# Performance work log

Hardware: AMD Instinct MI355X
Metric: run time of the kernel (lower is better)

The kernel has to match this reference:

```python
import jax, jax.numpy as jnp
import numpy as np

L = 4096
E = 512   # embed dim
S = 1024  # state dim
H = 150   # Scorer hidden dim
GI = 2 * S + E
MAX_N = 10


def _scorer(x, W1, b1, W2, b2, W3, b3):
    h = jax.nn.relu(x @ W1 + b1)
    h = jax.nn.relu(h @ W2 + b2)
    return h @ W3 + b3  # [..., 1]


def setup_inputs() -> dict:
    key = jax.random.key(0)
    ks = jax.random.split(key, 16)
    def init(k, shape, fan_in):
        return jax.random.normal(k, shape, dtype=jnp.float32) / np.sqrt(fan_in)
    inp = {
        "embeds": jax.random.normal(ks[0], (L, E), dtype=jnp.float32),
        "states": jax.random.normal(ks[1], (L, S), dtype=jnp.float32),
        # attention Scorer params (input S)
        "aW1": init(ks[2], (S, H), S), "ab1": jnp.zeros((H,), jnp.float32),
        "aW2": init(ks[3], (H, H), H), "ab2": jnp.zeros((H,), jnp.float32),
        "aW3": init(ks[4], (H, 1), H), "ab3": jnp.zeros((1,), jnp.float32),
        # sm Scorer params (input GI)
        "sW1": init(ks[5], (GI, H), GI), "sb1": jnp.zeros((H,), jnp.float32),
        "sW2": init(ks[6], (H, H), H), "sb2": jnp.zeros((H,), jnp.float32),
        "sW3": init(ks[7], (H, 1), H), "sb3": jnp.zeros((1,), jnp.float32),
    }
    return inp


def reference(embeds, states, aW1, ab1, aW2, ab2, aW3, ab3,
              sW1, sb1, sW2, sb2, sW3, sb3):
    # per-token attention logits, computed once: [L]
    attns = _scorer(states, aW1, ab1, aW2, ab2, aW3, ab3)[:, 0]

    gs = []
    for n in range(1, MAX_N + 1):  # fixed small loop over window sizes
        M = L - n + 1                                  # number of windows
        starts = jnp.arange(M)
        idx = starts[:, None] + jnp.arange(n)          # [M, n] token indices
        w = jax.nn.softmax(attns[idx], axis=1)         # windowed softmax [M, n]
        pooled = jnp.einsum('mn,mne->me', w, embeds[idx])  # [M, E]
        g = jnp.concatenate([states[starts], states[starts + n - 1], pooled],
                            axis=1)                    # [M, 2S+E]
        gs.append(g)
    x = jnp.concatenate(gs, axis=0)                    # [T, GI], T = 10L-45
    scores = _scorer(x, sW1, sb1, sW2, sb2, sW3, sb3)[:, 0]  # [T]
    return scores
```

## Files before the change

kernel.cpp:

```cpp
#include <hip/hip_runtime.h>
#include <math.h>

#define LTOK 4096
#define EDIM 512
#define SDIM 1024
#define HDIM 150
#define SEG 160
#define MAXN 10
#define TOTAL_ROWS 40915
#define KA 1536
#define NKT 48
#define K2 160
#define NCG 42

typedef _Float16 hfrag __attribute__((ext_vector_type(8)));
typedef float ffrag __attribute__((ext_vector_type(4)));

#define MFMA_(a, b, c) __builtin_amdgcn_mfma_f32_16x16x32_f16(a, b, c, 0, 0, 0)


#define ITEMS_A   (LTOK * (KA / 8))
#define ITEMS_W   (NCG * NKT * 64)
#define ITEMS_W2  (K2 * (K2 / 8))
#define ITEMS_A2  (K2 * (K2 / 8))
#define ITEMS_TOT (ITEMS_A + ITEMS_W + ITEMS_W2 + ITEMS_A2)

__global__ __launch_bounds__(256) void prep_kernel(
    const float* __restrict__ embeds, const float* __restrict__ states,
    const float* __restrict__ aW1, const float* __restrict__ aW2,
    const float* __restrict__ sW1, const float* __restrict__ sW2,
    _Float16* __restrict__ Apk, _Float16* __restrict__ Wpk,
    _Float16* __restrict__ W2pk, _Float16* __restrict__ A2pk)
{
    int it = blockIdx.x * 256 + threadIdx.x;
    if (it < ITEMS_A) {
        const int rem = it % (NKT * 64);
        const int g = it / (NKT * 64), kt = rem >> 6, lane = rem & 63;
        const int row = g * 16 + (lane & 15);
        const int k0 = kt * 32 + (lane >> 4) * 8;
        const float* src = (k0 < SDIM) ? (states + (size_t)row * SDIM + k0)
                                       : (embeds + (size_t)row * EDIM + (k0 - SDIM));
        const float4 v0 = *(const float4*)src;
        const float4 v1 = *(const float4*)(src + 4);
        _Float16 o[8] = {(_Float16)v0.x, (_Float16)v0.y, (_Float16)v0.z, (_Float16)v0.w,
                         (_Float16)v1.x, (_Float16)v1.y, (_Float16)v1.z, (_Float16)v1.w};
        *(uint4*)(Apk + (size_t)it * 8) = *(uint4*)o;
        return;
    }
    it -= ITEMS_A;
    if (it < ITEMS_W) {
        const int rem = it % (NKT * 64);
        const int cgi = it / (NKT * 64), kt = rem >> 6, lane = rem & 63;
        const int col = cgi * 16 + (lane & 15);
        const int k0 = kt * 32 + (lane >> 4) * 8;
        _Float16 o[8];
        for (int j = 0; j < 8; ++j) {
            const int k = k0 + j;
            float wv = 0.f;
            if (col < 160) {
                if (col < HDIM && k < SDIM) wv = sW1[(size_t)k * HDIM + col];
            } else if (col < 320) {
                const int cj = col - 160;
                if (cj < HDIM && k < SDIM) wv = sW1[(size_t)(SDIM + k) * HDIM + cj];
            } else if (col < 480) {
                const int cj = col - 320;
                if (cj < HDIM && k >= SDIM) wv = sW1[(size_t)(SDIM + k) * HDIM + cj];
            } else if (col >= 512) {
                const int cj = col - 512;
                if (cj < HDIM && k < SDIM) wv = aW1[(size_t)k * HDIM + cj];
            }
            o[j] = (_Float16)wv;
        }
        *(uint4*)(Wpk + ((size_t)((size_t)cgi * NKT + kt) * 64 + lane) * 8) = *(uint4*)o;
        return;
    }
    it -= ITEMS_W;
    if (it < ITEMS_W2 + ITEMS_A2) {
        const bool is_a = (it >= ITEMS_W2);
        const int li = is_a ? (it - ITEMS_W2) : it;
        const float* src = is_a ? aW2 : sW2;
        _Float16* dst = is_a ? A2pk : W2pk;
        const int tk = li >> 6, lane = li & 63;
        const int col = (tk / 5) * 16 + (lane & 15);
        const int k0 = (tk % 5) * 32 + (lane >> 4) * 8;
        _Float16 o[8];
        for (int j = 0; j < 8; ++j) {
            const int k = k0 + j;
            float wv = (col < HDIM && k < HDIM) ? src[(size_t)k * HDIM + col] : 0.f;
            o[j] = (_Float16)wv;
        }
        *(uint4*)(dst + ((size_t)tk * 64 + lane) * 8) = *(uint4*)o;
    }
}

__global__ __launch_bounds__(256) void k_proj(
    const _Float16* __restrict__ Apk, const _Float16* __restrict__ Wpk,
    const _Float16* __restrict__ A2pk,
    const float* __restrict__ ab1, const float* __restrict__ ab2,
    const float* __restrict__ aW3, const float* __restrict__ ab3,
    _Float16* __restrict__ P1h, _Float16* __restrict__ P2h,
    _Float16* __restrict__ PEh, float* __restrict__ attns)
{
    const int bid = blockIdx.x;
    const int tid = threadIdx.x;
    const int w = tid >> 6, lane = tid & 63;
    const int quad = lane >> 4, l16 = lane & 15;

    __shared__ __align__(16) _Float16 ah1[64 * SEG];

    if (bid % 9 == 0) {
        const int tok0 = (bid / 9) * 64;
        const int g = tok0 / 16 + w;

        ffrag acc[10];
#pragma unroll
        for (int c = 0; c < 10; ++c) acc[c] = (ffrag){0.f, 0.f, 0.f, 0.f};

        const _Float16* ap = Apk + ((size_t)g * NKT) * 512 + lane * 8;
        const _Float16* wb = Wpk + lane * 8;

#define LDA_(kt) (*(const hfrag*)(ap + (size_t)(kt) * 512))
#define LOADC(BX, kt, h)                                                    \
        _Pragma("unroll")                                                   \
        for (int c_ = 0; c_ < 5; ++c_)                                      \
            BX[c_] = *(const hfrag*)(wb +                                   \
                ((size_t)(32 + (h) * 5 + c_) * NKT + (kt)) * 512);
#define MFMA5(av, BX, h)                                                    \
        _Pragma("unroll")                                                   \
        for (int c_ = 0; c_ < 5; ++c_)                                      \
            acc[(h) * 5 + c_] = MFMA_(av, BX[c_], acc[(h) * 5 + c_]);

        hfrag aA = LDA_(0), aB;
        hfrag bX[5], bY[5];
        LOADC(bX, 0, 0);
        for (int kt = 0; kt < 32; ++kt) {
            LOADC(bY, kt, 1);
            if (kt + 1 < 32) aB = LDA_(kt + 1);
            MFMA5(aA, bX, 0);
            if (kt + 1 < 32) LOADC(bX, kt + 1, 0);
            MFMA5(aA, bY, 1);
            aA = aB;
        }
#undef LDA_
#undef LOADC
#undef MFMA5

#pragma unroll
        for (int c = 0; c < 10; ++c) {
            const int col = c * 16 + l16;
            const float b1 = (col < HDIM) ? ab1[col] : 0.f;
#pragma unroll
            for (int r = 0; r < 4; ++r) {
                const int row = w * 16 + quad * 4 + r;
                ah1[row * SEG + col] = (_Float16)fmaxf(acc[c][r] + b1, 0.f);
            }
        }
        __syncthreads();

        hfrag af[5];
#pragma unroll
        for (int ks = 0; ks < 5; ++ks)
            af[ks] = *(const hfrag*)&ah1[(w * 16 + l16) * SEG + ks * 32 + quad * 8];

        float part[4] = {0.f, 0.f, 0.f, 0.f};
        for (int ct = 0; ct < 10; ++ct) {
            ffrag a2 = (ffrag){0.f, 0.f, 0.f, 0.f};
#pragma unroll
            for (int ks = 0; ks < 5; ++ks) {
                const hfrag fb = *(const hfrag*)(
                    A2pk + ((size_t)(ct * 5 + ks) * 64 + lane) * 8);
                a2 = __builtin_amdgcn_mfma_f32_16x16x32_f16(af[ks], fb, a2, 0, 0, 0);
            }
            const int col = ct * 16 + l16;
            const float s2 = (col < HDIM) ? ab2[col] : 0.f;
            const float s3 = (col < HDIM) ? aW3[col] : 0.f;
#pragma unroll
            for (int r = 0; r < 4; ++r) part[r] += fmaxf(a2[r] + s2, 0.f) * s3;
        }
#pragma unroll
        for (int off = 1; off < 16; off <<= 1) {
#pragma unroll
            for (int r = 0; r < 4; ++r) part[r] += __shfl_xor(part[r], off, 64);
        }
        if (l16 == 0) {
            const float b3 = ab3[0];
#pragma unroll
            for (int r = 0; r < 4; ++r)
                attns[tok0 + w * 16 + quad * 4 + r] = part[r] + b3;
        }
        return;
    }

    const int tile = bid - bid / 9 - 1;
    const int bM = tile & 63, bN = tile >> 6;
    const int wm = w & 1, wn = w >> 1;
    const int gbase = bM * 4 + wm * 2;
    const int cgbase = bN * 4 + wn * 2;
    if (cgbase >= 30) return;
    const int kt0 = (bN >= 5) ? 32 : 0;
    const int kt1 = (bN >= 5) ? 48 : 32;

    ffrag acc[2][2];
#pragma unroll
    for (int t = 0; t < 2; ++t)
#pragma unroll
        for (int u = 0; u < 2; ++u) acc[t][u] = (ffrag){0.f, 0.f, 0.f, 0.f};

    const _Float16* a0p = Apk + ((size_t)(gbase + 0) * NKT) * 512 + lane * 8;
    const _Float16* a1p = Apk + ((size_t)(gbase + 1) * NKT) * 512 + lane * 8;
    const _Float16* b0p = Wpk + ((size_t)(cgbase + 0) * NKT) * 512 + lane * 8;
    const _Float16* b1p = Wpk + ((size_t)(cgbase + 1) * NKT) * 512 + lane * 8;

    hfrag Ax0[2], Ax1[2], Bx0[2], Bx1[2];
    hfrag Ay0[2], Ay1[2], By0[2], By1[2];

#define LOADB(A0_, A1_, B0_, B1_, kb)                                       \
    _Pragma("unroll")                                                       \
    for (int u_ = 0; u_ < 2; ++u_) {                                        \
        A0_[u_] = *(const hfrag*)(a0p + (size_t)((kb) + u_) * 512);         \
        A1_[u_] = *(const hfrag*)(a1p + (size_t)((kb) + u_) * 512);         \
        B0_[u_] = *(const hfrag*)(b0p + (size_t)((kb) + u_) * 512);         \
        B1_[u_] = *(const hfrag*)(b1p + (size_t)((kb) + u_) * 512);         \
    }
#define MFMAB(A0_, A1_, B0_, B1_)                                           \
    _Pragma("unroll")                                                       \
    for (int u_ = 0; u_ < 2; ++u_) {                                        \
        acc[0][0] = MFMA_(A0_[u_], B0_[u_], acc[0][0]);                     \
        acc[1][0] = MFMA_(A1_[u_], B0_[u_], acc[1][0]);                     \
        acc[0][1] = MFMA_(A0_[u_], B1_[u_], acc[0][1]);                     \
        acc[1][1] = MFMA_(A1_[u_], B1_[u_], acc[1][1]);                     \
    }

    LOADB(Ax0, Ax1, Bx0, Bx1, kt0);
    for (int kb = kt0; kb < kt1; kb += 4) {
        LOADB(Ay0, Ay1, By0, By1, kb + 2);
        MFMAB(Ax0, Ax1, Bx0, Bx1);
        if (kb + 4 < kt1) LOADB(Ax0, Ax1, Bx0, Bx1, kb + 4);
        MFMAB(Ay0, Ay1, By0, By1);
    }
#undef LOADB
#undef MFMAB

#pragma unroll
    for (int t = 0; t < 2; ++t)
#pragma unroll
        for (int u = 0; u < 2; ++u) {
            const int col = (cgbase + u) * 16 + l16;
#pragma unroll
            for (int r = 0; r < 4; ++r) {
                const int row = (gbase + t) * 16 + quad * 4 + r;
                const _Float16 hv = (_Float16)acc[t][u][r];
                if (col < 160)      P1h[(size_t)row * SEG + col] = hv;
                else if (col < 320) P2h[(size_t)row * SEG + (col - 160)] = hv;
                else if (col < 480) PEh[(size_t)row * SEG + (col - 320)] = hv;
            }
        }
}

__global__ __launch_bounds__(256) void span_kernel(
    const float* __restrict__ attns, const _Float16* __restrict__ P1h,
    const _Float16* __restrict__ P2h, const _Float16* __restrict__ PEh,
    const float* __restrict__ sb1, const _Float16* __restrict__ W2pk,
    const float* __restrict__ sb2, const float* __restrict__ sW3,
    const float* __restrict__ sb3, float* __restrict__ out)
{
    const int pairI = blockIdx.x % 5;
    const int mChunk = blockIdx.x / 5;
    const int n0 = 2 * pairI + 1, n1 = n0 + 1;
    const int Mn0 = LTOK - n0 + 1, Mn1 = Mn0 - 1;
    const int m0 = mChunk * 32;
    const int offn0 = (n0 - 1) * LTOK - ((n0 - 1) * (n0 - 2)) / 2;
    const int offn1 = offn0 + Mn0;

    const int tid = threadIdx.x;
    const int w = tid >> 6, lane = tid & 63, quad = lane >> 4, l16 = lane & 15;

    __shared__ __align__(16) _Float16 h1h[2][32 * K2];
    __shared__ __align__(16) _Float16 PEs[41 * SEG];
    __shared__ float wgt[2][32][MAXN];

    for (int t = tid; t < 41 * (SEG / 8); t += 256) {
        const int rr = t / (SEG / 8), cc = t % (SEG / 8);
        const int srcRow = min(m0 + rr, LTOK - 1);
        *(uint4*)&PEs[rr * SEG + cc * 8] =
            *(const uint4*)(PEh + (size_t)srcRow * SEG + cc * 8);
    }

    if (tid < 64) {
        const int q = tid >> 5, r = tid & 31;
        const int n = q ? n1 : n0;
        const int Mn = q ? Mn1 : Mn0;
        const int m = m0 + r;
        if (m < Mn) {
            float av[MAXN];
#pragma unroll
            for (int j = 0; j < MAXN; ++j)
                av[j] = attns[min(m + j, LTOK - 1)];
            float mx = -1e30f;
            for (int j = 0; j < n; ++j) mx = fmaxf(mx, av[j]);
            float tp[MAXN]; float s = 0.f;
            for (int j = 0; j < n; ++j) { tp[j] = expf(av[j] - mx); s += tp[j]; }
            const float inv = 1.f / s;
            for (int j = 0; j < MAXN; ++j) wgt[q][r][j] = (j < n) ? tp[j] * inv : 0.f;
        } else {
            for (int j = 0; j < MAXN; ++j) wgt[q][r][j] = 0.f;
        }
    }
    __syncthreads();

    for (int item = tid; item < 32 * (K2 / 8); item += 256) {
        const int r = item / (K2 / 8), cc = item % (K2 / 8);
        const int c0 = cc * 8;
        const int mm = m0 + r;
        const hfrag p1  = *(const hfrag*)(P1h + (size_t)mm * SEG + c0);
        const hfrag p2a = *(const hfrag*)(P2h + (size_t)min(mm + n0 - 1, LTOK - 1) * SEG + c0);
        const hfrag p2b = *(const hfrag*)(P2h + (size_t)min(mm + n0, LTOK - 1) * SEG + c0);
        float b1v[8];
#pragma unroll
        for (int e = 0; e < 8; ++e)
            b1v[e] = (c0 + e < HDIM) ? sb1[c0 + e] : 0.f;
        float a0[8], a1[8];
#pragma unroll
        for (int e = 0; e < 8; ++e) {
            a0[e] = (float)p1[e] + (float)p2a[e] + b1v[e];
            a1[e] = (float)p1[e] + (float)p2b[e] + b1v[e];
        }
#pragma unroll
        for (int j = 0; j < MAXN; ++j) {
            const hfrag pe = *(const hfrag*)&PEs[(r + j) * SEG + c0];
            const float w0j = wgt[0][r][j];
            const float w1j = wgt[1][r][j];
#pragma unroll
            for (int e = 0; e < 8; ++e) {
                const float pv = (float)pe[e];
                a0[e] = fmaf(w0j, pv, a0[e]);
                a1[e] = fmaf(w1j, pv, a1[e]);
            }
        }
        _Float16 o0[8], o1[8];
#pragma unroll
        for (int e = 0; e < 8; ++e) {
            const bool live = (c0 + e < HDIM);
            o0[e] = live ? (_Float16)fmaxf(a0[e], 0.f) : (_Float16)0.f;
            o1[e] = live ? (_Float16)fmaxf(a1[e], 0.f) : (_Float16)0.f;
        }
        *(uint4*)&h1h[0][r * K2 + c0] = *(uint4*)o0;
        *(uint4*)&h1h[1][r * K2 + c0] = *(uint4*)o1;
    }
    __syncthreads();

    const int q = w >> 1, rg = w & 1;
    const int Mq = q ? Mn1 : Mn0;
    const int offq = q ? offn1 : offn0;

    hfrag af[5];
#pragma unroll
    for (int ks = 0; ks < 5; ++ks)
        af[ks] = *(const hfrag*)&h1h[q][(rg * 16 + l16) * K2 + ks * 32 + quad * 8];

    float part[4] = {0.f, 0.f, 0.f, 0.f};
    for (int ct = 0; ct < 10; ++ct) {
        ffrag acc = (ffrag){0.f, 0.f, 0.f, 0.f};
#pragma unroll
        for (int ks = 0; ks < 5; ++ks) {
            const hfrag fb = *(const hfrag*)(
                W2pk + ((size_t)(ct * 5 + ks) * 64 + lane) * 8);
            acc = __builtin_amdgcn_mfma_f32_16x16x32_f16(af[ks], fb, acc, 0, 0, 0);
        }
        const int col = ct * 16 + l16;
        const float s2 = (col < HDIM) ? sb2[col] : 0.f;
        const float s3 = (col < HDIM) ? sW3[col] : 0.f;
#pragma unroll
        for (int r = 0; r < 4; ++r) part[r] += fmaxf(acc[r] + s2, 0.f) * s3;
    }

#pragma unroll
    for (int off = 1; off < 16; off <<= 1) {
#pragma unroll
        for (int r = 0; r < 4; ++r) part[r] += __shfl_xor(part[r], off, 64);
    }
    if (l16 == 0) {
        const float b3 = sb3[0];
#pragma unroll
        for (int r = 0; r < 4; ++r) {
            const int lr = rg * 16 + quad * 4 + r;
            if (m0 + lr < Mq) out[offq + m0 + lr] = part[r] + b3;
        }
    }
}

extern "C" void kernel_launch(void* const* d_in, const int* in_sizes, int n_in,
                              void* d_out, int out_size, void* d_ws, size_t ws_size,
                              hipStream_t stream) {
    const float* embeds = (const float*)d_in[0];
    const float* states = (const float*)d_in[1];
    const float* aW1 = (const float*)d_in[2];
    const float* ab1 = (const float*)d_in[3];
    const float* aW2 = (const float*)d_in[4];
    const float* ab2 = (const float*)d_in[5];
    const float* aW3 = (const float*)d_in[6];
    const float* ab3 = (const float*)d_in[7];
    const float* sW1 = (const float*)d_in[8];
    const float* sb1 = (const float*)d_in[9];
    const float* sW2 = (const float*)d_in[10];
    const float* sb2 = (const float*)d_in[11];
    const float* sW3 = (const float*)d_in[12];
    const float* sb3 = (const float*)d_in[13];
    float* out = (float*)d_out;

    float* attns = (float*)d_ws;
    _Float16* P1h  = (_Float16*)(attns + LTOK);
    _Float16* P2h  = P1h + (size_t)LTOK * SEG;
    _Float16* PEh  = P2h + (size_t)LTOK * SEG;
    _Float16* Apk  = PEh + (size_t)LTOK * SEG;
    _Float16* Wpk  = Apk + (size_t)ITEMS_A * 8;
    _Float16* W2pk = Wpk + (size_t)ITEMS_W * 8;
    _Float16* A2pk = W2pk + (size_t)ITEMS_W2 * 8;

    prep_kernel<<<ITEMS_TOT / 256, 256, 0, stream>>>(
        embeds, states, aW1, aW2, sW1, sW2, Apk, Wpk, W2pk, A2pk);
    k_proj<<<576, 256, 0, stream>>>(
        Apk, Wpk, A2pk, ab1, ab2, aW3, ab3, P1h, P2h, PEh, attns);
    span_kernel<<<640, 256, 0, stream>>>(
        attns, P1h, P2h, PEh, sb1, W2pk, sb2, sW3, sb3, out);
}
```

Measured before the change: 144.6 us.

## Enlarge k_proj GEMM wave tiles to 4x4 MFMA blocks and shrink grid

Each wave in the k_proj projection GEMM now computes a 64x64 output tile (4x4 MFMA fragments) instead of 32x32 (2x2). This raises operand reuse per loaded fragment and cuts redundant global/L2 traffic. The grid drops from 576 to 192 blocks, and the attention-scorer blocks now come first as a contiguous range instead of being interleaved every ninth block. The trade-offs are more accumulator registers per wave and fewer waves than CUs, so parallelism and latency hiding drop. Two unused column groups (30 and 31) are also computed and then discarded at store time.

```diff
diff --git a/kernel.cpp b/kernel.cpp
--- a/kernel.cpp
+++ b/kernel.cpp
@@ -108,8 +108,8 @@
 
     __shared__ __align__(16) _Float16 ah1[64 * SEG];
 
-    if (bid % 9 == 0) {
-        const int tok0 = (bid / 9) * 64;
+    if (bid < 64) {
+        const int tok0 = bid * 64;
         const int g = tok0 / 16 + w;
 
         ffrag acc[10];
@@ -191,60 +191,52 @@
         return;
     }
 
-    const int tile = bid - bid / 9 - 1;
-    const int bM = tile & 63, bN = tile >> 6;
-    const int wm = w & 1, wn = w >> 1;
-    const int gbase = bM * 4 + wm * 2;
-    const int cgbase = bN * 4 + wn * 2;
-    if (cgbase >= 30) return;
-    const int kt0 = (bN >= 5) ? 32 : 0;
-    const int kt1 = (bN >= 5) ? 48 : 32;
-
-    ffrag acc[2][2];
-#pragma unroll
-    for (int t = 0; t < 2; ++t)
-#pragma unroll
-        for (int u = 0; u < 2; ++u) acc[t][u] = (ffrag){0.f, 0.f, 0.f, 0.f};
-
-    const _Float16* a0p = Apk + ((size_t)(gbase + 0) * NKT) * 512 + lane * 8;
-    const _Float16* a1p = Apk + ((size_t)(gbase + 1) * NKT) * 512 + lane * 8;
-    const _Float16* b0p = Wpk + ((size_t)(cgbase + 0) * NKT) * 512 + lane * 8;
-    const _Float16* b1p = Wpk + ((size_t)(cgbase + 1) * NKT) * 512 + lane * 8;
-
-    hfrag Ax0[2], Ax1[2], Bx0[2], Bx1[2];
-    hfrag Ay0[2], Ay1[2], By0[2], By1[2];
-
-#define LOADB(A0_, A1_, B0_, B1_, kb)                                       \
+    const int mb = bid - 64;
+    const int bM = mb & 63;
+    const int bH = mb >> 6;
+    const int gbase = bM * 4;
+    const int cgbase = bH * 16 + w * 4;
+    const int kt0 = (cgbase >= 20) ? 32 : 0;
+    const int kt1 = (cgbase >= 20) ? 48 : 32;
+
+    ffrag acc[4][4];
+#pragma unroll
+    for (int t = 0; t < 4; ++t)
+#pragma unroll
+        for (int u = 0; u < 4; ++u) acc[t][u] = (ffrag){0.f, 0.f, 0.f, 0.f};
+
+    const _Float16* aB = Apk + ((size_t)gbase * NKT) * 512 + lane * 8;
+    const _Float16* bB = Wpk + ((size_t)cgbase * NKT) * 512 + lane * 8;
+
+    hfrag AX[4], BX[4], AY[4], BY[4];
+
+#define LDSET(AS_, BS_, kt)                                                 \
     _Pragma("unroll")                                                       \
-    for (int u_ = 0; u_ < 2; ++u_) {                                        \
-        A0_[u_] = *(const hfrag*)(a0p + (size_t)((kb) + u_) * 512);         \
-        A1_[u_] = *(const hfrag*)(a1p + (size_t)((kb) + u_) * 512);         \
-        B0_[u_] = *(const hfrag*)(b0p + (size_t)((kb) + u_) * 512);         \
-        B1_[u_] = *(const hfrag*)(b1p + (size_t)((kb) + u_) * 512);         \
-    }
-#define MFMAB(A0_, A1_, B0_, B1_)                                           \
+    for (int g_ = 0; g_ < 4; ++g_) {                                        \
+        AS_[g_] = *(const hfrag*)(aB + ((size_t)g_ * NKT + (kt)) * 512);    \
+        BS_[g_] = *(const hfrag*)(bB + ((size_t)g_ * NKT + (kt)) * 512);    \
+    }
+#define MFMASET(AS_, BS_)                                                   \
     _Pragma("unroll")                                                       \
-    for (int u_ = 0; u_ < 2; ++u_) {                                        \
-        acc[0][0] = MFMA_(A0_[u_], B0_[u_], acc[0][0]);                     \
-        acc[1][0] = MFMA_(A1_[u_], B0_[u_], acc[1][0]);                     \
-        acc[0][1] = MFMA_(A0_[u_], B1_[u_], acc[0][1]);                     \
-        acc[1][1] = MFMA_(A1_[u_], B1_[u_], acc[1][1]);                     \
-    }
-
-    LOADB(Ax0, Ax1, Bx0, Bx1, kt0);
-    for (int kb = kt0; kb < kt1; kb += 4) {
-        LOADB(Ay0, Ay1, By0, By1, kb + 2);
-        MFMAB(Ax0, Ax1, Bx0, Bx1);
-        if (kb + 4 < kt1) LOADB(Ax0, Ax1, Bx0, Bx1, kb + 4);
-        MFMAB(Ay0, Ay1, By0, By1);
-    }
-#undef LOADB
-#undef MFMAB
-
-#pragma unroll
-    for (int t = 0; t < 2; ++t)
-#pragma unroll
-        for (int u = 0; u < 2; ++u) {
+    for (int t_ = 0; t_ < 4; ++t_)                                          \
+        _Pragma("unroll")                                                   \
+        for (int u_ = 0; u_ < 4; ++u_)                                      \
+            acc[t_][u_] = MFMA_(AS_[t_], BS_[u_], acc[t_][u_]);
+
+    LDSET(AX, BX, kt0);
+    for (int kt = kt0; kt < kt1; kt += 2) {
+        LDSET(AY, BY, kt + 1);
+        MFMASET(AX, BX);
+        if (kt + 2 < kt1) LDSET(AX, BX, kt + 2);
+        MFMASET(AY, BY);
+    }
+#undef LDSET
+#undef MFMASET
+
+#pragma unroll
+    for (int t = 0; t < 4; ++t)
+#pragma unroll
+        for (int u = 0; u < 4; ++u) {
             const int col = (cgbase + u) * 16 + l16;
 #pragma unroll
             for (int r = 0; r < 4; ++r) {
@@ -419,7 +411,7 @@
 
     prep_kernel<<<ITEMS_TOT / 256, 256, 0, stream>>>(
         embeds, states, aW1, aW2, sW1, sW2, Apk, Wpk, W2pk, A2pk);
-    k_proj<<<576, 256, 0, stream>>>(
+    k_proj<<<192, 256, 0, stream>>>(
         Apk, Wpk, A2pk, ab1, ab2, aW3, ab3, P1h, P2h, PEh, attns);
     span_kernel<<<640, 256, 0, stream>>>(
         attns, P1h, P2h, PEh, sb1, W2pk, sb2, sW3, sb3, out);
```

New measurement: 143.7 us. No clear change (-0.6%).

## Fuse prep, projection and span kernels into one persistent kernel with grid barriers

Applied to the files above, without the earlier changes.

Merges the three kernel launches into a single 640-block kernel. Two software grid barriers, built on an atomic counter in workspace that is reset with a memset, separate the packing, projection and span phases. Shared memory is shared across phases through a union. The aim is to remove the launch gaps and tail drain between kernels, at the cost of relying on all 640 blocks being co-resident, spin-wait barrier overhead, and a memset call before each launch.

```diff
diff --git a/kernel.cpp b/kernel.cpp
--- a/kernel.cpp
+++ b/kernel.cpp
@@ -12,6 +12,7 @@
 #define NKT 48
 #define K2 160
 #define NCG 42
+#define NBLK 640
 
 typedef _Float16 hfrag __attribute__((ext_vector_type(8)));
 typedef float ffrag __attribute__((ext_vector_type(4)));
@@ -25,14 +26,27 @@
 #define ITEMS_A2  (K2 * (K2 / 8))
 #define ITEMS_TOT (ITEMS_A + ITEMS_W + ITEMS_W2 + ITEMS_A2)
 
-__global__ __launch_bounds__(256) void prep_kernel(
+__device__ __forceinline__ void grid_barrier(int* cnt, int tid) {
+    __syncthreads();
+    if (tid == 0) {
+        __threadfence();
+        __hip_atomic_fetch_add(cnt, 1, __ATOMIC_RELAXED, __HIP_MEMORY_SCOPE_AGENT);
+        while (__hip_atomic_load(cnt, __ATOMIC_RELAXED, __HIP_MEMORY_SCOPE_AGENT)
+               < NBLK)
+            __builtin_amdgcn_s_sleep(2);
+        __threadfence();
+    }
+    __syncthreads();
+}
+
+__device__ __forceinline__ void prep_item(
+    int it,
     const float* __restrict__ embeds, const float* __restrict__ states,
     const float* __restrict__ aW1, const float* __restrict__ aW2,
     const float* __restrict__ sW1, const float* __restrict__ sW2,
     _Float16* __restrict__ Apk, _Float16* __restrict__ Wpk,
     _Float16* __restrict__ W2pk, _Float16* __restrict__ A2pk)
 {
-    int it = blockIdx.x * 256 + threadIdx.x;
     if (it < ITEMS_A) {
         const int rem = it % (NKT * 64);
         const int g = it / (NKT * 64), kt = rem >> 6, lane = rem & 63;
@@ -93,23 +107,43 @@
     }
 }
 
-__global__ __launch_bounds__(256) void k_proj(
-    const _Float16* __restrict__ Apk, const _Float16* __restrict__ Wpk,
-    const _Float16* __restrict__ A2pk,
-    const float* __restrict__ ab1, const float* __restrict__ ab2,
+union SMem {
+    _Float16 ah1[64 * SEG];
+    struct {
+        _Float16 h1h[2][32 * K2];
+        _Float16 PEs[41 * SEG];
+        float wgt[2][32][MAXN];
+    } sp;
+};
+
+__global__ __launch_bounds__(256, 4) void fused_kernel(
+    const float* __restrict__ embeds, const float* __restrict__ states,
+    const float* __restrict__ aW1, const float* __restrict__ ab1,
+    const float* __restrict__ aW2, const float* __restrict__ ab2,
     const float* __restrict__ aW3, const float* __restrict__ ab3,
+    const float* __restrict__ sW1, const float* __restrict__ sb1,
+    const float* __restrict__ sW2, const float* __restrict__ sb2,
+    const float* __restrict__ sW3, const float* __restrict__ sb3,
+    _Float16* __restrict__ Apk, _Float16* __restrict__ Wpk,
+    _Float16* __restrict__ W2pk, _Float16* __restrict__ A2pk,
     _Float16* __restrict__ P1h, _Float16* __restrict__ P2h,
-    _Float16* __restrict__ PEh, float* __restrict__ attns)
+    _Float16* __restrict__ PEh, float* __restrict__ attns,
+    float* __restrict__ out, int* bar)
 {
     const int bid = blockIdx.x;
     const int tid = threadIdx.x;
     const int w = tid >> 6, lane = tid & 63;
     const int quad = lane >> 4, l16 = lane & 15;
 
-    __shared__ __align__(16) _Float16 ah1[64 * SEG];
-
-    if (bid % 9 == 0) {
-        const int tok0 = (bid / 9) * 64;
+    __shared__ __align__(16) SMem sm;
+
+    for (int it = bid * 256 + tid; it < ITEMS_TOT; it += NBLK * 256)
+        prep_item(it, embeds, states, aW1, aW2, sW1, sW2, Apk, Wpk, W2pk, A2pk);
+
+    grid_barrier(&bar[0], tid);
+
+    if (bid < 64) {
+        const int tok0 = bid * 64;
         const int g = tok0 / 16 + w;
 
         ffrag acc[10];
@@ -152,7 +186,7 @@
 #pragma unroll
             for (int r = 0; r < 4; ++r) {
                 const int row = w * 16 + quad * 4 + r;
-                ah1[row * SEG + col] = (_Float16)fmaxf(acc[c][r] + b1, 0.f);
+                sm.ah1[row * SEG + col] = (_Float16)fmaxf(acc[c][r] + b1, 0.f);
             }
         }
         __syncthreads();
@@ -160,7 +194,7 @@
         hfrag af[5];
 #pragma unroll
         for (int ks = 0; ks < 5; ++ks)
-            af[ks] = *(const hfrag*)&ah1[(w * 16 + l16) * SEG + ks * 32 + quad * 8];
+            af[ks] = *(const hfrag*)&sm.ah1[(w * 16 + l16) * SEG + ks * 32 + quad * 8];
 
         float part[4] = {0.f, 0.f, 0.f, 0.f};
         for (int ct = 0; ct < 10; ++ct) {
@@ -169,7 +203,7 @@
             for (int ks = 0; ks < 5; ++ks) {
                 const hfrag fb = *(const hfrag*)(
                     A2pk + ((size_t)(ct * 5 + ks) * 64 + lane) * 8);
-                a2 = __builtin_amdgcn_mfma_f32_16x16x32_f16(af[ks], fb, a2, 0, 0, 0);
+                a2 = MFMA_(af[ks], fb, a2);
             }
             const int col = ct * 16 + l16;
             const float s2 = (col < HDIM) ? ab2[col] : 0.f;
@@ -188,203 +222,193 @@
             for (int r = 0; r < 4; ++r)
                 attns[tok0 + w * 16 + quad * 4 + r] = part[r] + b3;
         }
-        return;
-    }
-
-    const int tile = bid - bid / 9 - 1;
-    const int bM = tile & 63, bN = tile >> 6;
-    const int wm = w & 1, wn = w >> 1;
-    const int gbase = bM * 4 + wm * 2;
-    const int cgbase = bN * 4 + wn * 2;
-    if (cgbase >= 30) return;
-    const int kt0 = (bN >= 5) ? 32 : 0;
-    const int kt1 = (bN >= 5) ? 48 : 32;
-
-    ffrag acc[2][2];
-#pragma unroll
-    for (int t = 0; t < 2; ++t)
-#pragma unroll
-        for (int u = 0; u < 2; ++u) acc[t][u] = (ffrag){0.f, 0.f, 0.f, 0.f};
-
-    const _Float16* a0p = Apk + ((size_t)(gbase + 0) * NKT) * 512 + lane * 8;
-    const _Float16* a1p = Apk + ((size_t)(gbase + 1) * NKT) * 512 + lane * 8;
-    const _Float16* b0p = Wpk + ((size_t)(cgbase + 0) * NKT) * 512 + lane * 8;
-    const _Float16* b1p = Wpk + ((size_t)(cgbase + 1) * NKT) * 512 + lane * 8;
-
-    hfrag Ax0[2], Ax1[2], Bx0[2], Bx1[2];
-    hfrag Ay0[2], Ay1[2], By0[2], By1[2];
+    } else if (bid < 576) {
+        const int tile = bid - 64;
+        const int bM = tile & 63, bN = tile >> 6;
+        const int wm = w & 1, wn = w >> 1;
+        const int gbase = bM * 4 + wm * 2;
+        const int cgbase = bN * 4 + wn * 2;
+        if (cgbase < 30) {
+            const int kt0 = (bN >= 5) ? 32 : 0;
+            const int kt1 = (bN >= 5) ? 48 : 32;
+
+            ffrag acc[2][2];
+#pragma unroll
+            for (int t = 0; t < 2; ++t)
+#pragma unroll
+                for (int u = 0; u < 2; ++u) acc[t][u] = (ffrag){0.f, 0.f, 0.f, 0.f};
+
+            const _Float16* a0p = Apk + ((size_t)(gbase + 0) * NKT) * 512 + lane * 8;
+            const _Float16* a1p = Apk + ((size_t)(gbase + 1) * NKT) * 512 + lane * 8;
+            const _Float16* b0p = Wpk + ((size_t)(cgbase + 0) * NKT) * 512 + lane * 8;
+            const _Float16* b1p = Wpk + ((size_t)(cgbase + 1) * NKT) * 512 + lane * 8;
+
+            hfrag Ax0[2], Ax1[2], Bx0[2], Bx1[2];
+            hfrag Ay0[2], Ay1[2], By0[2], By1[2];
 
 #define LOADB(A0_, A1_, B0_, B1_, kb)                                       \
-    _Pragma("unroll")                                                       \
-    for (int u_ = 0; u_ < 2; ++u_) {                                        \
-        A0_[u_] = *(const hfrag*)(a0p + (size_t)((kb) + u_) * 512);         \
-        A1_[u_] = *(const hfrag*)(a1p + (size_t)((kb) + u_) * 512);         \
-        B0_[u_] = *(const hfrag*)(b0p + (size_t)((kb) + u_) * 512);         \
-        B1_[u_] = *(const hfrag*)(b1p + (size_t)((kb) + u_) * 512);         \
-    }
+            _Pragma("unroll")                                               \
+            for (int u_ = 0; u_ < 2; ++u_) {                                \
+                A0_[u_] = *(const hfrag*)(a0p + (size_t)((kb) + u_) * 512); \
+                A1_[u_] = *(const hfrag*)(a1p + (size_t)((kb) + u_) * 512); \
+                B0_[u_] = *(const hfrag*)(b0p + (size_t)((kb) + u_) * 512); \
+                B1_[u_] = *(const hfrag*)(b1p + (size_t)((kb) + u_) * 512); \
+            }
 #define MFMAB(A0_, A1_, B0_, B1_)                                           \
-    _Pragma("unroll")                                                       \
-    for (int u_ = 0; u_ < 2; ++u_) {                                        \
-        acc[0][0] = MFMA_(A0_[u_], B0_[u_], acc[0][0]);                     \
-        acc[1][0] = MFMA_(A1_[u_], B0_[u_], acc[1][0]);                     \
-        acc[0][1] = MFMA_(A0_[u_], B1_[u_], acc[0][1]);                     \
-        acc[1][1] = MFMA_(A1_[u_], B1_[u_], acc[1][1]);                     \
-    }
-
-    LOADB(Ax0, Ax1, Bx0, Bx1, kt0);
-    for (int kb = kt0; kb < kt1; kb += 4) {
-        LOADB(Ay0, Ay1, By0, By1, kb + 2);
-        MFMAB(Ax0, Ax1, Bx0, Bx1);
-        if (kb + 4 < kt1) LOADB(Ax0, Ax1, Bx0, Bx1, kb + 4);
-        MFMAB(Ay0, Ay1, By0, By1);
-    }
+            _Pragma("unroll")                                               \
+            for (int u_ = 0; u_ < 2; ++u_) {                                \
+                acc[0][0] = MFMA_(A0_[u_], B0_[u_], acc[0][0]);             \
+                acc[1][0] = MFMA_(A1_[u_], B0_[u_], acc[1][0]);             \
+                acc[0][1] = MFMA_(A0_[u_], B1_[u_], acc[0][1]);             \
+                acc[1][1] = MFMA_(A1_[u_], B1_[u_], acc[1][1]);             \
+            }
+
+            LOADB(Ax0, Ax1, Bx0, Bx1, kt0);
+            for (int kb = kt0; kb < kt1; kb += 4) {
+                LOADB(Ay0, Ay1, By0, By1, kb + 2);
+                MFMAB(Ax0, Ax1, Bx0, Bx1);
+                if (kb + 4 < kt1) LOADB(Ax0, Ax1, Bx0, Bx1, kb + 4);
+                MFMAB(Ay0, Ay1, By0, By1);
+            }
 #undef LOADB
 #undef MFMAB
 
 #pragma unroll
-    for (int t = 0; t < 2; ++t)
-#pragma unroll
-        for (int u = 0; u < 2; ++u) {
-            const int col = (cgbase + u) * 16 + l16;
+            for (int t = 0; t < 2; ++t)
+#pragma unroll
+                for (int u = 0; u < 2; ++u) {
+                    const int col = (cgbase + u) * 16 + l16;
+#pragma unroll
+                    for (int r = 0; r < 4; ++r) {
+                        const int row = (gbase + t) * 16 + quad * 4 + r;
+                        const _Float16 hv = (_Float16)acc[t][u][r];
+                        if (col < 160)      P1h[(size_t)row * SEG + col] = hv;
+                        else if (col < 320) P2h[(size_t)row * SEG + (col - 160)] = hv;
+                        else if (col < 480) PEh[(size_t)row * SEG + (col - 320)] = hv;
+                    }
+                }
+        }
+    }
+
+    grid_barrier(&bar[1], tid);
+
+    {
+        const int pairI = bid % 5;
+        const int mChunk = bid / 5;
+        const int n0 = 2 * pairI + 1, n1 = n0 + 1;
+        const int Mn0 = LTOK - n0 + 1, Mn1 = Mn0 - 1;
+        const int m0 = mChunk * 32;
+        const int offn0 = (n0 - 1) * LTOK - ((n0 - 1) * (n0 - 2)) / 2;
+        const int offn1 = offn0 + Mn0;
+
+        for (int t = tid; t < 41 * (SEG / 8); t += 256) {
+            const int rr = t / (SEG / 8), cc = t % (SEG / 8);
+            const int srcRow = min(m0 + rr, LTOK - 1);
+            *(uint4*)&sm.sp.PEs[rr * SEG + cc * 8] =
+                *(const uint4*)(PEh + (size_t)srcRow * SEG + cc * 8);
+        }
+
+        if (tid < 64) {
+            const int q = tid >> 5, r = tid & 31;
+            const int n = q ? n1 : n0;
+            const int Mn = q ? Mn1 : Mn0;
+            const int m = m0 + r;
+            if (m < Mn) {
+                float av[MAXN];
+#pragma unroll
+                for (int j = 0; j < MAXN; ++j)
+                    av[j] = attns[min(m + j, LTOK - 1)];
+                float mx = -1e30f;
+                for (int j = 0; j < n; ++j) mx = fmaxf(mx, av[j]);
+                float tp[MAXN]; float s = 0.f;
+                for (int j = 0; j < n; ++j) { tp[j] = expf(av[j] - mx); s += tp[j]; }
+                const float inv = 1.f / s;
+                for (int j = 0; j < MAXN; ++j)
+                    sm.sp.wgt[q][r][j] = (j < n) ? tp[j] * inv : 0.f;
+            } else {
+                for (int j = 0; j < MAXN; ++j) sm.sp.wgt[q][r][j] = 0.f;
+            }
+        }
+        __syncthreads();
+
+        for (int item = tid; item < 32 * (K2 / 8); item += 256) {
+            const int r = item / (K2 / 8), cc = item % (K2 / 8);
+            const int c0 = cc * 8;
+            const int mm = m0 + r;
+            const hfrag p1  = *(const hfrag*)(P1h + (size_t)mm * SEG + c0);
+            const hfrag p2a = *(const hfrag*)(P2h + (size_t)min(mm + n0 - 1, LTOK - 1) * SEG + c0);
+            const hfrag p2b = *(const hfrag*)(P2h + (size_t)min(mm + n0, LTOK - 1) * SEG + c0);
+            float b1v[8];
+#pragma unroll
+            for (int e = 0; e < 8; ++e)
+                b1v[e] = (c0 + e < HDIM) ? sb1[c0 + e] : 0.f;
+            float a0[8], a1[8];
+#pragma unroll
+            for (int e = 0; e < 8; ++e) {
+                a0[e] = (float)p1[e] + (float)p2a[e] + b1v[e];
+                a1[e] = (float)p1[e] + (float)p2b[e] + b1v[e];
+            }
+#pragma unroll
+            for (int j = 0; j < MAXN; ++j) {
+                const hfrag pe = *(const hfrag*)&sm.sp.PEs[(r + j) * SEG + c0];
+                const float w0j = sm.sp.wgt[0][r][j];
+                const float w1j = sm.sp.wgt[1][r][j];
+#pragma unroll
+                for (int e = 0; e < 8; ++e) {
+                    const float pv = (float)pe[e];
+                    a0[e] = fmaf(w0j, pv, a0[e]);
+                    a1[e] = fmaf(w1j, pv, a1[e]);
+                }
+            }
+            _Float16 o0[8], o1[8];
+#pragma unroll
+            for (int e = 0; e < 8; ++e) {
+                const bool live = (c0 + e < HDIM);
+                o0[e] = live ? (_Float16)fmaxf(a0[e], 0.f) : (_Float16)0.f;
+                o1[e] = live ? (_Float16)fmaxf(a1[e], 0.f) : (_Float16)0.f;
+            }
+            *(uint4*)&sm.sp.h1h[0][r * K2 + c0] = *(uint4*)o0;
+            *(uint4*)&sm.sp.h1h[1][r * K2 + c0] = *(uint4*)o1;
+        }
+        __syncthreads();
+
+        const int q = w >> 1, rg = w & 1;
+        const int Mq = q ? Mn1 : Mn0;
+        const int offq = q ? offn1 : offn0;
+
+        hfrag af[5];
+#pragma unroll
+        for (int ks = 0; ks < 5; ++ks)
+            af[ks] = *(const hfrag*)&sm.sp.h1h[q][(rg * 16 + l16) * K2 + ks * 32 + quad * 8];
+
+        float part[4] = {0.f, 0.f, 0.f, 0.f};
+        for (int ct = 0; ct < 10; ++ct) {
+            ffrag acc = (ffrag){0.f, 0.f, 0.f, 0.f};
+#pragma unroll
+            for (int ks = 0; ks < 5; ++ks) {
+                const hfrag fb = *(const hfrag*)(
+                    W2pk + ((size_t)(ct * 5 + ks) * 64 + lane) * 8);
+                acc = MFMA_(af[ks], fb, acc);
+            }
+            const int col = ct * 16 + l16;
+            const float s2 = (col < HDIM) ? sb2[col] : 0.f;
+            const float s3 = (col < HDIM) ? sW3[col] : 0.f;
+#pragma unroll
+            for (int r = 0; r < 4; ++r) part[r] += fmaxf(acc[r] + s2, 0.f) * s3;
+        }
+
+#pragma unroll
+        for (int off = 1; off < 16; off <<= 1) {
+#pragma unroll
+            for (int r = 0; r < 4; ++r) part[r] += __shfl_xor(part[r], off, 64);
+        }
+        if (l16 == 0) {
+            const float b3 = sb3[0];
 #pragma unroll
             for (int r = 0; r < 4; ++r) {
-                const int row = (gbase + t) * 16 + quad * 4 + r;
-                const _Float16 hv = (_Float16)acc[t][u][r];
-                if (col < 160)      P1h[(size_t)row * SEG + col] = hv;
-                else if (col < 320) P2h[(size_t)row * SEG + (col - 160)] = hv;
-                else if (col < 480) PEh[(size_t)row * SEG + (col - 320)] = hv;
-            }
-        }
-}
-
-__global__ __launch_bounds__(256) void span_kernel(
-    const float* __restrict__ attns, const _Float16* __restrict__ P1h,
-    const _Float16* __restrict__ P2h, const _Float16* __restrict__ PEh,
-    const float* __restrict__ sb1, const _Float16* __restrict__ W2pk,
-    const float* __restrict__ sb2, const float* __restrict__ sW3,
-    const float* __restrict__ sb3, float* __restrict__ out)
-{
-    const int pairI = blockIdx.x % 5;
-    const int mChunk = blockIdx.x / 5;
-    const int n0 = 2 * pairI + 1, n1 = n0 + 1;
-    const int Mn0 = LTOK - n0 + 1, Mn1 = Mn0 - 1;
-    const int m0 = mChunk * 32;
-    const int offn0 = (n0 - 1) * LTOK - ((n0 - 1) * (n0 - 2)) / 2;
-    const int offn1 = offn0 + Mn0;
-
-    const int tid = threadIdx.x;
-    const int w = tid >> 6, lane = tid & 63, quad = lane >> 4, l16 = lane & 15;
-
-    __shared__ __align__(16) _Float16 h1h[2][32 * K2];
-    __shared__ __align__(16) _Float16 PEs[41 * SEG];
-    __shared__ float wgt[2][32][MAXN];
-
-    for (int t = tid; t < 41 * (SEG / 8); t += 256) {
-        const int rr = t / (SEG / 8), cc = t % (SEG / 8);
-        const int srcRow = min(m0 + rr, LTOK - 1);
-        *(uint4*)&PEs[rr * SEG + cc * 8] =
-            *(const uint4*)(PEh + (size_t)srcRow * SEG + cc * 8);
-    }
-
-    if (tid < 64) {
-        const int q = tid >> 5, r = tid & 31;
-        const int n = q ? n1 : n0;
-        const int Mn = q ? Mn1 : Mn0;
-        const int m = m0 + r;
-        if (m < Mn) {
-            float av[MAXN];
-#pragma unroll
-            for (int j = 0; j < MAXN; ++j)
-                av[j] = attns[min(m + j, LTOK - 1)];
-            float mx = -1e30f;
-            for (int j = 0; j < n; ++j) mx = fmaxf(mx, av[j]);
-            float tp[MAXN]; float s = 0.f;
-            for (int j = 0; j < n; ++j) { tp[j] = expf(av[j] - mx); s += tp[j]; }
-            const float inv = 1.f / s;
-            for (int j = 0; j < MAXN; ++j) wgt[q][r][j] = (j < n) ? tp[j] * inv : 0.f;
-        } else {
-            for (int j = 0; j < MAXN; ++j) wgt[q][r][j] = 0.f;
-        }
-    }
-    __syncthreads();
-
-    for (int item = tid; item < 32 * (K2 / 8); item += 256) {
-        const int r = item / (K2 / 8), cc = item % (K2 / 8);
-        const int c0 = cc * 8;
-        const int mm = m0 + r;
-        const hfrag p1  = *(const hfrag*)(P1h + (size_t)mm * SEG + c0);
-        const hfrag p2a = *(const hfrag*)(P2h + (size_t)min(mm + n0 - 1, LTOK - 1) * SEG + c0);
-        const hfrag p2b = *(const hfrag*)(P2h + (size_t)min(mm + n0, LTOK - 1) * SEG + c0);
-        float b1v[8];
-#pragma unroll
-        for (int e = 0; e < 8; ++e)
-            b1v[e] = (c0 + e < HDIM) ? sb1[c0 + e] : 0.f;
-        float a0[8], a1[8];
-#pragma unroll
-        for (int e = 0; e < 8; ++e) {
-            a0[e] = (float)p1[e] + (float)p2a[e] + b1v[e];
-            a1[e] = (float)p1[e] + (float)p2b[e] + b1v[e];
-        }
-#pragma unroll
-        for (int j = 0; j < MAXN; ++j) {
-            const hfrag pe = *(const hfrag*)&PEs[(r + j) * SEG + c0];
-            const float w0j = wgt[0][r][j];
-            const float w1j = wgt[1][r][j];
-#pragma unroll
-            for (int e = 0; e < 8; ++e) {
-                const float pv = (float)pe[e];
-                a0[e] = fmaf(w0j, pv, a0[e]);
-                a1[e] = fmaf(w1j, pv, a1[e]);
-            }
-        }
-        _Float16 o0[8], o1[8];
-#pragma unroll
-        for (int e = 0; e < 8; ++e) {
-            const bool live = (c0 + e < HDIM);
-            o0[e] = live ? (_Float16)fmaxf(a0[e], 0.f) : (_Float16)0.f;
-            o1[e] = live ? (_Float16)fmaxf(a1[e], 0.f) : (_Float16)0.f;
-        }
-        *(uint4*)&h1h[0][r * K2 + c0] = *(uint4*)o0;
-        *(uint4*)&h1h[1][r * K2 + c0] = *(uint4*)o1;
-    }
-    __syncthreads();
-
-    const int q = w >> 1, rg = w & 1;
-    const int Mq = q ? Mn1 : Mn0;
-    const int offq = q ? offn1 : offn0;
-
-    hfrag af[5];
-#pragma unroll
-    for (int ks = 0; ks < 5; ++ks)
-        af[ks] = *(const hfrag*)&h1h[q][(rg * 16 + l16) * K2 + ks * 32 + quad * 8];
-
-    float part[4] = {0.f, 0.f, 0.f, 0.f};
-    for (int ct = 0; ct < 10; ++ct) {
-        ffrag acc = (ffrag){0.f, 0.f, 0.f, 0.f};
-#pragma unroll
-        for (int ks = 0; ks < 5; ++ks) {
-            const hfrag fb = *(const hfrag*)(
-                W2pk + ((size_t)(ct * 5 + ks) * 64 + lane) * 8);
-            acc = __builtin_amdgcn_mfma_f32_16x16x32_f16(af[ks], fb, acc, 0, 0, 0);
-        }
-        const int col = ct * 16 + l16;
-        const float s2 = (col < HDIM) ? sb2[col] : 0.f;
-        const float s3 = (col < HDIM) ? sW3[col] : 0.f;
-#pragma unroll
-        for (int r = 0; r < 4; ++r) part[r] += fmaxf(acc[r] + s2, 0.f) * s3;
-    }
-
-#pragma unroll
-    for (int off = 1; off < 16; off <<= 1) {
-#pragma unroll
-        for (int r = 0; r < 4; ++r) part[r] += __shfl_xor(part[r], off, 64);
-    }
-    if (l16 == 0) {
-        const float b3 = sb3[0];
-#pragma unroll
-        for (int r = 0; r < 4; ++r) {
-            const int lr = rg * 16 + quad * 4 + r;
-            if (m0 + lr < Mq) out[offq + m0 + lr] = part[r] + b3;
+                const int lr = rg * 16 + quad * 4 + r;
+                if (m0 + lr < Mq) out[offq + m0 + lr] = part[r] + b3;
+            }
         }
     }
 }
@@ -416,11 +440,11 @@
     _Float16* Wpk  = Apk + (size_t)ITEMS_A * 8;
     _Float16* W2pk = Wpk + (size_t)ITEMS_W * 8;
     _Float16* A2pk = W2pk + (size_t)ITEMS_W2 * 8;
-
-    prep_kernel<<<ITEMS_TOT / 256, 256, 0, stream>>>(
-        embeds, states, aW1, aW2, sW1, sW2, Apk, Wpk, W2pk, A2pk);
-    k_proj<<<576, 256, 0, stream>>>(
-        Apk, Wpk, A2pk, ab1, ab2, aW3, ab3, P1h, P2h, PEh, attns);
-    span_kernel<<<640, 256, 0, stream>>>(
-        attns, P1h, P2h, PEh, sb1, W2pk, sb2, sW3, sb3, out);
+    int* bar       = (int*)(A2pk + (size_t)ITEMS_A2 * 8);
+
+    hipMemsetAsync(bar, 0, 2 * sizeof(int), stream);
+    fused_kernel<<<NBLK, 256, 0, stream>>>(
+        embeds, states, aW1, ab1, aW2, ab2, aW3, ab3,
+        sW1, sb1, sW2, sb2, sW3, sb3,
+        Apk, Wpk, W2pk, A2pk, P1h, P2h, PEh, attns, out, bar);
 }
```

After: 308.3 us. 2.13x slower.

## Fold attention layer-1 into tiled projection GEMM and recompute attention logits in span kernel

Applied to the files above, without the earlier changes.

Removes the special attention blocks (every ninth block) from k_proj, which ran a long per-wave serial K loop. The attention-scorer first layer now runs as extra column tiles of the regular 2x2-fragment GEMM, and its ReLU output is written to a new fp16 workspace buffer. Layers 2 and 3 of the attention scorer are now computed inside span_kernel for the 48 tokens each block needs, reading from shared memory. This balances the load in k_proj. In exchange, span blocks redundantly recompute the attention MLP for overlapping token ranges, add an extra sync, and write and read an extra intermediate buffer.

```diff
diff --git a/kernel.cpp b/kernel.cpp
--- a/kernel.cpp
+++ b/kernel.cpp
@@ -95,110 +95,23 @@
 
 __global__ __launch_bounds__(256) void k_proj(
     const _Float16* __restrict__ Apk, const _Float16* __restrict__ Wpk,
-    const _Float16* __restrict__ A2pk,
-    const float* __restrict__ ab1, const float* __restrict__ ab2,
-    const float* __restrict__ aW3, const float* __restrict__ ab3,
+    const float* __restrict__ ab1,
     _Float16* __restrict__ P1h, _Float16* __restrict__ P2h,
-    _Float16* __restrict__ PEh, float* __restrict__ attns)
+    _Float16* __restrict__ PEh, _Float16* __restrict__ AH1h)
 {
     const int bid = blockIdx.x;
     const int tid = threadIdx.x;
     const int w = tid >> 6, lane = tid & 63;
     const int quad = lane >> 4, l16 = lane & 15;
 
-    __shared__ __align__(16) _Float16 ah1[64 * SEG];
-
-    if (bid % 9 == 0) {
-        const int tok0 = (bid / 9) * 64;
-        const int g = tok0 / 16 + w;
-
-        ffrag acc[10];
-#pragma unroll
-        for (int c = 0; c < 10; ++c) acc[c] = (ffrag){0.f, 0.f, 0.f, 0.f};
-
-        const _Float16* ap = Apk + ((size_t)g * NKT) * 512 + lane * 8;
-        const _Float16* wb = Wpk + lane * 8;
-
-#define LDA_(kt) (*(const hfrag*)(ap + (size_t)(kt) * 512))
-#define LOADC(BX, kt, h)                                                    \
-        _Pragma("unroll")                                                   \
-        for (int c_ = 0; c_ < 5; ++c_)                                      \
-            BX[c_] = *(const hfrag*)(wb +                                   \
-                ((size_t)(32 + (h) * 5 + c_) * NKT + (kt)) * 512);
-#define MFMA5(av, BX, h)                                                    \
-        _Pragma("unroll")                                                   \
-        for (int c_ = 0; c_ < 5; ++c_)                                      \
-            acc[(h) * 5 + c_] = MFMA_(av, BX[c_], acc[(h) * 5 + c_]);
-
-        hfrag aA = LDA_(0), aB;
-        hfrag bX[5], bY[5];
-        LOADC(bX, 0, 0);
-        for (int kt = 0; kt < 32; ++kt) {
-            LOADC(bY, kt, 1);
-            if (kt + 1 < 32) aB = LDA_(kt + 1);
-            MFMA5(aA, bX, 0);
-            if (kt + 1 < 32) LOADC(bX, kt + 1, 0);
-            MFMA5(aA, bY, 1);
-            aA = aB;
-        }
-#undef LDA_
-#undef LOADC
-#undef MFMA5
-
-#pragma unroll
-        for (int c = 0; c < 10; ++c) {
-            const int col = c * 16 + l16;
-            const float b1 = (col < HDIM) ? ab1[col] : 0.f;
-#pragma unroll
-            for (int r = 0; r < 4; ++r) {
-                const int row = w * 16 + quad * 4 + r;
-                ah1[row * SEG + col] = (_Float16)fmaxf(acc[c][r] + b1, 0.f);
-            }
-        }
-        __syncthreads();
-
-        hfrag af[5];
-#pragma unroll
-        for (int ks = 0; ks < 5; ++ks)
-            af[ks] = *(const hfrag*)&ah1[(w * 16 + l16) * SEG + ks * 32 + quad * 8];
-
-        float part[4] = {0.f, 0.f, 0.f, 0.f};
-        for (int ct = 0; ct < 10; ++ct) {
-            ffrag a2 = (ffrag){0.f, 0.f, 0.f, 0.f};
-#pragma unroll
-            for (int ks = 0; ks < 5; ++ks) {
-                const hfrag fb = *(const hfrag*)(
-                    A2pk + ((size_t)(ct * 5 + ks) * 64 + lane) * 8);
-                a2 = __builtin_amdgcn_mfma_f32_16x16x32_f16(af[ks], fb, a2, 0, 0, 0);
-            }
-            const int col = ct * 16 + l16;
-            const float s2 = (col < HDIM) ? ab2[col] : 0.f;
-            const float s3 = (col < HDIM) ? aW3[col] : 0.f;
-#pragma unroll
-            for (int r = 0; r < 4; ++r) part[r] += fmaxf(a2[r] + s2, 0.f) * s3;
-        }
-#pragma unroll
-        for (int off = 1; off < 16; off <<= 1) {
-#pragma unroll
-            for (int r = 0; r < 4; ++r) part[r] += __shfl_xor(part[r], off, 64);
-        }
-        if (l16 == 0) {
-            const float b3 = ab3[0];
-#pragma unroll
-            for (int r = 0; r < 4; ++r)
-                attns[tok0 + w * 16 + quad * 4 + r] = part[r] + b3;
-        }
-        return;
-    }
-
-    const int tile = bid - bid / 9 - 1;
-    const int bM = tile & 63, bN = tile >> 6;
+    const int bM = bid & 63, bN = bid >> 6;
     const int wm = w & 1, wn = w >> 1;
     const int gbase = bM * 4 + wm * 2;
-    const int cgbase = bN * 4 + wn * 2;
-    if (cgbase >= 30) return;
-    const int kt0 = (bN >= 5) ? 32 : 0;
-    const int kt1 = (bN >= 5) ? 48 : 32;
+    const int cgl = bN * 4 + wn * 2;
+    const int cga0 = cgl + ((cgl >= 30) ? 2 : 0);
+    const int cga1 = (cgl + 1) + (((cgl + 1) >= 30) ? 2 : 0);
+    const int kt0 = (bN == 5 || bN == 6) ? 32 : 0;
+    const int kt1 = (bN >= 5 && bN <= 7) ? 48 : 32;
 
     ffrag acc[2][2];
 #pragma unroll
@@ -208,8 +121,8 @@
 
     const _Float16* a0p = Apk + ((size_t)(gbase + 0) * NKT) * 512 + lane * 8;
     const _Float16* a1p = Apk + ((size_t)(gbase + 1) * NKT) * 512 + lane * 8;
-    const _Float16* b0p = Wpk + ((size_t)(cgbase + 0) * NKT) * 512 + lane * 8;
-    const _Float16* b1p = Wpk + ((size_t)(cgbase + 1) * NKT) * 512 + lane * 8;
+    const _Float16* b0p = Wpk + ((size_t)cga0 * NKT) * 512 + lane * 8;
+    const _Float16* b1p = Wpk + ((size_t)cga1 * NKT) * 512 + lane * 8;
 
     hfrag Ax0[2], Ax1[2], Bx0[2], Bx1[2];
     hfrag Ay0[2], Ay1[2], By0[2], By1[2];
@@ -245,24 +158,35 @@
     for (int t = 0; t < 2; ++t)
 #pragma unroll
         for (int u = 0; u < 2; ++u) {
-            const int col = (cgbase + u) * 16 + l16;
+            const int cga = u ? cga1 : cga0;
 #pragma unroll
             for (int r = 0; r < 4; ++r) {
                 const int row = (gbase + t) * 16 + quad * 4 + r;
-                const _Float16 hv = (_Float16)acc[t][u][r];
-                if (col < 160)      P1h[(size_t)row * SEG + col] = hv;
-                else if (col < 320) P2h[(size_t)row * SEG + (col - 160)] = hv;
-                else if (col < 480) PEh[(size_t)row * SEG + (col - 320)] = hv;
+                if (cga < 30) {
+                    const int col = cga * 16 + l16;
+                    const _Float16 hv = (_Float16)acc[t][u][r];
+                    if (col < 160)      P1h[(size_t)row * SEG + col] = hv;
+                    else if (col < 320) P2h[(size_t)row * SEG + (col - 160)] = hv;
+                    else                PEh[(size_t)row * SEG + (col - 320)] = hv;
+                } else {
+                    const int colA = (cga - 32) * 16 + l16;
+                    const float b1 = (colA < HDIM) ? ab1[colA] : 0.f;
+                    AH1h[(size_t)row * SEG + colA] =
+                        (_Float16)fmaxf(acc[t][u][r] + b1, 0.f);
+                }
             }
         }
 }
 
 __global__ __launch_bounds__(256) void span_kernel(
-    const float* __restrict__ attns, const _Float16* __restrict__ P1h,
+    const _Float16* __restrict__ AH1h, const _Float16* __restrict__ P1h,
     const _Float16* __restrict__ P2h, const _Float16* __restrict__ PEh,
     const float* __restrict__ sb1, const _Float16* __restrict__ W2pk,
     const float* __restrict__ sb2, const float* __restrict__ sW3,
-    const float* __restrict__ sb3, float* __restrict__ out)
+    const float* __restrict__ sb3,
+    const _Float16* __restrict__ A2pk, const float* __restrict__ ab2,
+    const float* __restrict__ aW3, const float* __restrict__ ab3,
+    float* __restrict__ out)
 {
     const int pairI = blockIdx.x % 5;
     const int mChunk = blockIdx.x / 5;
@@ -277,6 +201,8 @@
 
     __shared__ __align__(16) _Float16 h1h[2][32 * K2];
     __shared__ __align__(16) _Float16 PEs[41 * SEG];
+    __shared__ __align__(16) _Float16 AH1s[48 * SEG];
+    __shared__ float att[48];
     __shared__ float wgt[2][32][MAXN];
 
     for (int t = tid; t < 41 * (SEG / 8); t += 256) {
@@ -285,6 +211,48 @@
         *(uint4*)&PEs[rr * SEG + cc * 8] =
             *(const uint4*)(PEh + (size_t)srcRow * SEG + cc * 8);
     }
+    for (int t = tid; t < 48 * (SEG / 8); t += 256) {
+        const int rr = t / (SEG / 8), cc = t % (SEG / 8);
+        const int srcRow = min(m0 + rr, LTOK - 1);
+        *(uint4*)&AH1s[rr * SEG + cc * 8] =
+            *(const uint4*)(AH1h + (size_t)srcRow * SEG + cc * 8);
+    }
+    __syncthreads();
+
+    if (w < 3) {
+        hfrag af[5];
+#pragma unroll
+        for (int ks = 0; ks < 5; ++ks)
+            af[ks] = *(const hfrag*)&AH1s[(w * 16 + l16) * SEG + ks * 32 + quad * 8];
+
+        float part[4] = {0.f, 0.f, 0.f, 0.f};
+        for (int ct = 0; ct < 10; ++ct) {
+            ffrag a2 = (ffrag){0.f, 0.f, 0.f, 0.f};
+#pragma unroll
+            for (int ks = 0; ks < 5; ++ks) {
+                const hfrag fb = *(const hfrag*)(
+                    A2pk + ((size_t)(ct * 5 + ks) * 64 + lane) * 8);
+                a2 = MFMA_(af[ks], fb, a2);
+            }
+            const int col = ct * 16 + l16;
+            const float s2 = (col < HDIM) ? ab2[col] : 0.f;
+            const float s3 = (col < HDIM) ? aW3[col] : 0.f;
+#pragma unroll
+            for (int r = 0; r < 4; ++r) part[r] += fmaxf(a2[r] + s2, 0.f) * s3;
+        }
+#pragma unroll
+        for (int off = 1; off < 16; off <<= 1) {
+#pragma unroll
+            for (int r = 0; r < 4; ++r) part[r] += __shfl_xor(part[r], off, 64);
+        }
+        if (l16 == 0) {
+            const float b3 = ab3[0];
+#pragma unroll
+            for (int r = 0; r < 4; ++r)
+                att[w * 16 + quad * 4 + r] = part[r] + b3;
+        }
+    }
+    __syncthreads();
 
     if (tid < 64) {
         const int q = tid >> 5, r = tid & 31;
@@ -292,10 +260,11 @@
         const int Mn = q ? Mn1 : Mn0;
         const int m = m0 + r;
         if (m < Mn) {
+            const int jcap = LTOK - 1 - m0;
             float av[MAXN];
 #pragma unroll
             for (int j = 0; j < MAXN; ++j)
-                av[j] = attns[min(m + j, LTOK - 1)];
+                av[j] = att[min(r + j, jcap)];
             float mx = -1e30f;
             for (int j = 0; j < n; ++j) mx = fmaxf(mx, av[j]);
             float tp[MAXN]; float s = 0.f;
@@ -353,38 +322,38 @@
     const int Mq = q ? Mn1 : Mn0;
     const int offq = q ? offn1 : offn0;
 
-    hfrag af[5];
+    hfrag af2[5];
 #pragma unroll
     for (int ks = 0; ks < 5; ++ks)
-        af[ks] = *(const hfrag*)&h1h[q][(rg * 16 + l16) * K2 + ks * 32 + quad * 8];
-
-    float part[4] = {0.f, 0.f, 0.f, 0.f};
+        af2[ks] = *(const hfrag*)&h1h[q][(rg * 16 + l16) * K2 + ks * 32 + quad * 8];
+
+    float part2[4] = {0.f, 0.f, 0.f, 0.f};
     for (int ct = 0; ct < 10; ++ct) {
         ffrag acc = (ffrag){0.f, 0.f, 0.f, 0.f};
 #pragma unroll
         for (int ks = 0; ks < 5; ++ks) {
             const hfrag fb = *(const hfrag*)(
                 W2pk + ((size_t)(ct * 5 + ks) * 64 + lane) * 8);
-            acc = __builtin_amdgcn_mfma_f32_16x16x32_f16(af[ks], fb, acc, 0, 0, 0);
+            acc = MFMA_(af2[ks], fb, acc);
         }
         const int col = ct * 16 + l16;
         const float s2 = (col < HDIM) ? sb2[col] : 0.f;
         const float s3 = (col < HDIM) ? sW3[col] : 0.f;
 #pragma unroll
-        for (int r = 0; r < 4; ++r) part[r] += fmaxf(acc[r] + s2, 0.f) * s3;
+        for (int r = 0; r < 4; ++r) part2[r] += fmaxf(acc[r] + s2, 0.f) * s3;
     }
 
 #pragma unroll
     for (int off = 1; off < 16; off <<= 1) {
 #pragma unroll
-        for (int r = 0; r < 4; ++r) part[r] += __shfl_xor(part[r], off, 64);
+        for (int r = 0; r < 4; ++r) part2[r] += __shfl_xor(part2[r], off, 64);
     }
     if (l16 == 0) {
         const float b3 = sb3[0];
 #pragma unroll
         for (int r = 0; r < 4; ++r) {
             const int lr = rg * 16 + quad * 4 + r;
-            if (m0 + lr < Mq) out[offq + m0 + lr] = part[r] + b3;
+            if (m0 + lr < Mq) out[offq + m0 + lr] = part2[r] + b3;
         }
     }
 }
@@ -408,19 +377,20 @@
     const float* sb3 = (const float*)d_in[13];
     float* out = (float*)d_out;
 
-    float* attns = (float*)d_ws;
-    _Float16* P1h  = (_Float16*)(attns + LTOK);
+    _Float16* P1h  = (_Float16*)d_ws;
     _Float16* P2h  = P1h + (size_t)LTOK * SEG;
     _Float16* PEh  = P2h + (size_t)LTOK * SEG;
-    _Float16* Apk  = PEh + (size_t)LTOK * SEG;
+    _Float16* AH1h = PEh + (size_t)LTOK * SEG;
+    _Float16* Apk  = AH1h + (size_t)LTOK * SEG;
     _Float16* Wpk  = Apk + (size_t)ITEMS_A * 8;
     _Float16* W2pk = Wpk + (size_t)ITEMS_W * 8;
     _Float16* A2pk = W2pk + (size_t)ITEMS_W2 * 8;
 
     prep_kernel<<<ITEMS_TOT / 256, 256, 0, stream>>>(
         embeds, states, aW1, aW2, sW1, sW2, Apk, Wpk, W2pk, A2pk);
-    k_proj<<<576, 256, 0, stream>>>(
-        Apk, Wpk, A2pk, ab1, ab2, aW3, ab3, P1h, P2h, PEh, attns);
+    k_proj<<<640, 256, 0, stream>>>(
+        Apk, Wpk, ab1, P1h, P2h, PEh, AH1h);
     span_kernel<<<640, 256, 0, stream>>>(
-        attns, P1h, P2h, PEh, sb1, W2pk, sb2, sW3, sb3, out);
+        AH1h, P1h, P2h, PEh, sb1, W2pk, sb2, sW3, sb3,
+        A2pk, ab2, aW3, ab3, out);
 }
```

Measured after the change: 144.9 us. About the same (+0.2%).
